# Kernel tuning notes

Hardware: AMD Instinct MI355X
Metric: run time of the kernel (lower is better)

Reference implementation:

```python
import jax, jax.numpy as jnp
import numpy as np

N = 25000      # nodes
E = 400000     # edges
D = 128        # num_hidden (per-head out dim)
H = 3          # heads
NEG_SLOPE = 0.2
BN_EPS = 1e-5


def _gatv2(x, edge_index, Wl, bl, Wr, br, att, bias):
    """PyG GATv2Conv (concat=True, add_self_loops=True, dropout=0).
    x: [N, Din]; Wl/Wr: [Din, H*D]; att: [H, D]; bias: [H*D].
    """
    n = x.shape[0]
    h, d = att.shape
    loops = jnp.arange(n)
    src = jnp.concatenate([edge_index[0], loops])  # [E+N]
    dst = jnp.concatenate([edge_index[1], loops])
    xl = (x @ Wl + bl).reshape(n, h, d)  # source transform
    xr = (x @ Wr + br).reshape(n, h, d)  # target transform
    # edge scores: a^T LeakyReLU(xl_j + xr_i)
    e = jax.nn.leaky_relu(xl[src] + xr[dst], NEG_SLOPE)   # [E+N, H, D]
    score = jnp.einsum('ehd,hd->eh', e, att)              # [E+N, H]
    # segment softmax over incoming edges of each dst node
    m = jax.ops.segment_max(score, dst, num_segments=n)   # [N, H]
    ex = jnp.exp(score - m[dst])
    denom = jax.ops.segment_sum(ex, dst, num_segments=n)  # [N, H]
    alpha = ex / denom[dst]                               # [E+N, H]
    out = jax.ops.segment_sum(alpha[:, :, None] * xl[src], dst, num_segments=n)
    return out.reshape(n, h * d) + bias                   # [N, H*D]


def _batchnorm(x, gamma, beta):
    mu = jnp.mean(x, axis=0)
    var = jnp.var(x, axis=0)  # biased, as torch BN uses for normalization
    return gamma * (x - mu) * jax.lax.rsqrt(var + BN_EPS) + beta


def setup_inputs() -> dict:
    key = jax.random.key(0)
    ks = iter(jax.random.split(key, 32))
    s = 0.1
    p = {}
    p['x'] = jax.random.normal(next(ks), (N, D), jnp.float32)
    p['edge_index'] = jax.random.randint(next(ks), (2, E), 0, N, jnp.int64)
    for i in (1, 2):
        p[f'Wl{i}'] = s * jax.random.normal(next(ks), (D, H * D), jnp.float32)
        p[f'bl{i}'] = jnp.zeros((H * D,), jnp.float32)
        p[f'Wr{i}'] = s * jax.random.normal(next(ks), (D, H * D), jnp.float32)
        p[f'br{i}'] = jnp.zeros((H * D,), jnp.float32)
        p[f'att{i}'] = s * jax.random.normal(next(ks), (H, D), jnp.float32)
        p[f'bc{i}'] = jnp.zeros((H * D,), jnp.float32)
        p[f'g{i}'] = jnp.ones((D,), jnp.float32)
        p[f'be{i}'] = jnp.zeros((D,), jnp.float32)
    p['W1'] = s * jax.random.normal(next(ks), (H * D, D), jnp.float32)
    p['b1'] = jnp.zeros((D,), jnp.float32)
    p['W2'] = s * jax.random.normal(next(ks), (2 * H * D, D), jnp.float32)
    p['b2'] = jnp.zeros((D,), jnp.float32)
    return p


def reference(x, edge_index, Wl1, bl1, Wr1, br1, att1, bc1, g1, be1,
              Wl2, bl2, Wr2, br2, att2, bc2, g2, be2, W1, b1, W2, b2):
    x_in = _gatv2(x, edge_index, Wl1, bl1, Wr1, br1, att1, bc1)  # [N, H*D]
    h = _batchnorm(x_in @ W1 + b1, g1, be1)
    h = jax.nn.relu(h)                                           # [N, D]
    h2 = _gatv2(h, edge_index, Wl2, bl2, Wr2, br2, att2, bc2)    # [N, H*D]
    out = jnp.concatenate([h2, x_in], axis=1) @ W2 + b2          # [N, D]
    out = _batchnorm(out, g2, be2)
    return jax.nn.relu(out)
```

## Files before the change

kernel.cpp:

```cpp
#include <hip/hip_runtime.h>
#include <math.h>

#define NN 25000
#define NE 400000
#define DD 128
#define HD 384
#define NEG 0.2f
#define EPS 1e-5f

typedef unsigned int u32;
typedef unsigned short u16;
typedef __attribute__((ext_vector_type(8))) short short8;
typedef __attribute__((ext_vector_type(4))) float floatx4;
typedef __attribute__((ext_vector_type(2))) float f32x2;

__device__ __forceinline__ u32 bf16_1(float x) {
    u32 u = __float_as_uint(x);
    return (u + 0x7fffu + ((u >> 16) & 1u)) >> 16;
}
__device__ __forceinline__ float blo(u32 u) { return __uint_as_float(u << 16); }
__device__ __forceinline__ float bhi(u32 u) { return __uint_as_float(u & 0xffff0000u); }

__device__ __forceinline__ void up8f2(uint4 u, f32x2* f) {
    f[0] = f32x2{blo(u.x), bhi(u.x)};
    f[1] = f32x2{blo(u.y), bhi(u.y)};
    f[2] = f32x2{blo(u.z), bhi(u.z)};
    f[3] = f32x2{blo(u.w), bhi(u.w)};
}

__device__ __forceinline__ f32x2 pk_add(f32x2 a, f32x2 b) {
    f32x2 d; asm("v_pk_add_f32 %0, %1, %2" : "=v"(d) : "v"(a), "v"(b)); return d;
}
__device__ __forceinline__ f32x2 pk_fma(f32x2 a, f32x2 b, f32x2 c) {
    f32x2 d; asm("v_pk_fma_f32 %0, %1, %2, %3" : "=v"(d) : "v"(a), "v"(b), "v"(c)); return d;
}
__device__ __forceinline__ f32x2 fabs2(f32x2 v) {
    u32 a = __float_as_uint(v.x) & 0x7fffffffu;
    u32 b = __float_as_uint(v.y) & 0x7fffffffu;
    return f32x2{__uint_as_float(a), __uint_as_float(b)};
}

__device__ __forceinline__ float row_sum16(float x) {
    int t;
    t = __builtin_amdgcn_update_dpp(0, __float_as_int(x), 0x121, 0xf, 0xf, false);
    x += __int_as_float(t);
    t = __builtin_amdgcn_update_dpp(0, __float_as_int(x), 0x122, 0xf, 0xf, false);
    x += __int_as_float(t);
    t = __builtin_amdgcn_update_dpp(0, __float_as_int(x), 0x124, 0xf, 0xf, false);
    x += __int_as_float(t);
    t = __builtin_amdgcn_update_dpp(0, __float_as_int(x), 0x128, 0xf, 0xf, false);
    x += __int_as_float(t);
    return x;
}

__global__ void k_cast_all(const float* __restrict__ x,
                           const float* __restrict__ Wl1, const float* __restrict__ Wr1,
                           const float* __restrict__ W1,
                           const float* __restrict__ Wl2, const float* __restrict__ Wr2,
                           const float* __restrict__ W2,
                           const float* __restrict__ bl1, const float* __restrict__ br1,
                           const float* __restrict__ bl2, const float* __restrict__ br2,
                           const float* __restrict__ att1, const float* __restrict__ att2,
                           const int* __restrict__ esrc, const int* __restrict__ edst,
                           u16* __restrict__ xb, u16* __restrict__ WfT1,
                           u16* __restrict__ W1T, u16* __restrict__ WfT2,
                           u16* __restrict__ W2T,
                           float* __restrict__ fb1, float* __restrict__ fb2,
                           float* __restrict__ attc1, float* __restrict__ attc2,
                           int* __restrict__ cnt, int* __restrict__ col_src,
                           float* __restrict__ stats) {
    int i = blockIdx.x * 256 + threadIdx.x;
    if (i < 400000) {
        const float4* xp = (const float4*)(x + (size_t)i * 8);
        float4 a = xp[0], b = xp[1];
        uint4 w;
        w.x = bf16_1(a.x) | (bf16_1(a.y) << 16);
        w.y = bf16_1(a.z) | (bf16_1(a.w) << 16);
        w.z = bf16_1(b.x) | (bf16_1(b.y) << 16);
        w.w = bf16_1(b.z) | (bf16_1(b.w) << 16);
        *(uint4*)(xb + (size_t)i * 8) = w;
        return;
    }
    i -= 400000;
    if (i < 400000) {
        int d = edst[i];
        int p = atomicAdd(&cnt[d], 1);
        col_src[(d << 6) + p] = esrc[i];
        return;
    }
    i -= 400000;
    if (i < 49152) { int k = i / 384, n = i - k * 384; WfT1[n * 128 + k] = (u16)bf16_1(Wl1[i]); return; }
    i -= 49152;
    if (i < 49152) { int k = i / 384, n = i - k * 384; WfT1[(384 + n) * 128 + k] = (u16)bf16_1(Wr1[i]); return; }
    i -= 49152;
    if (i < 49152) { int k = i / 128, n = i - k * 128; W1T[n * 384 + k] = (u16)bf16_1(W1[i]); return; }
    i -= 49152;
    if (i < 49152) { int k = i / 384, n = i - k * 384; WfT2[n * 128 + k] = (u16)bf16_1(Wl2[i]); return; }
    i -= 49152;
    if (i < 49152) { int k = i / 384, n = i - k * 384; WfT2[(384 + n) * 128 + k] = (u16)bf16_1(Wr2[i]); return; }
    i -= 49152;
    if (i < 98304) { int k = i / 128, n = i - k * 128; W2T[n * 768 + k] = (u16)bf16_1(W2[i]); return; }
    i -= 98304;
    if (i < 768) { fb1[i] = (i < 384) ? bl1[i] : br1[i - 384]; return; }
    i -= 768;
    if (i < 768) { fb2[i] = (i < 384) ? bl2[i] : br2[i - 384]; return; }
    i -= 768;
    if (i < 384) { attc1[i] = att1[i] * 0.86561702f; return; }
    i -= 384;
    if (i < 384) { attc2[i] = att2[i] * 0.86561702f; return; }
    i -= 384;
    if (i < 512) stats[i] = 0.f;
}
#define CAST_TOTAL (400000 + 400000 + 5 * 49152 + 98304 + 1536 + 768 + 512)

__global__ __launch_bounds__(256) void k_gemm_k128(
        const u16* __restrict__ A, const u16* __restrict__ BT,
        const float* __restrict__ bias, u16* __restrict__ Cb, int M) {
    __shared__ short sA[64 * 128];
    __shared__ short sB[128 * 128];
    int tid = threadIdx.x;
    int wv = tid >> 6, lane = tid & 63;
    int quad = lane >> 4, m16 = lane & 15;
    int mb = blockIdx.x * 64;

#pragma unroll
    for (int j = 0; j < 4; ++j) {
        int L = j * 256 + tid;
        int r = L >> 4, c8 = (L & 15) ^ (r & 15);
        int gr = mb + r; gr = gr < M ? gr : M - 1;
        __builtin_amdgcn_global_load_lds(
            (const __attribute__((address_space(1))) void*)(A + (size_t)gr * 128 + c8 * 8),
            (__attribute__((address_space(3))) void*)(sA + (size_t)L * 8), 16, 0, 0);
    }

    for (int nb6 = 0; nb6 < 6; ++nb6) {
        int nb = nb6 * 128;
        __syncthreads();
#pragma unroll
        for (int j = 0; j < 8; ++j) {
            int L = j * 256 + tid;
            int r = L >> 4, c8 = (L & 15) ^ (r & 15);
            __builtin_amdgcn_global_load_lds(
                (const __attribute__((address_space(1))) void*)(BT + (size_t)(nb + r) * 128 + c8 * 8),
                (__attribute__((address_space(3))) void*)(sB + (size_t)L * 8), 16, 0, 0);
        }
        __syncthreads();

        floatx4 acc[8];
#pragma unroll
        for (int nf = 0; nf < 8; ++nf)
#pragma unroll
            for (int r = 0; r < 4; ++r) acc[nf][r] = 0.f;

#pragma unroll
        for (int ks = 0; ks < 4; ++ks) {
            int slot = (ks * 4 + quad) ^ m16;
            short8 a0 = *(const short8*)(sA + ((size_t)(wv * 16 + m16) * 16 + slot) * 8);
#pragma unroll
            for (int nf = 0; nf < 8; ++nf) {
                short8 b = *(const short8*)(sB + ((size_t)(nf * 16 + m16) * 16 + slot) * 8);
                acc[nf] = __builtin_amdgcn_mfma_f32_16x16x32_bf16(a0, b, acc[nf], 0, 0, 0);
            }
        }
        __syncthreads();

#pragma unroll
        for (int nf = 0; nf < 8; ++nf)
#pragma unroll
            for (int r = 0; r < 4; ++r) {
                int row = wv * 16 + quad * 4 + r;
                int col = nf * 16 + m16;
                sB[row * 128 + col] = (short)bf16_1(acc[nf][r] + bias[nb + col]);
            }
        __syncthreads();

        int xr = nb >= 384;
        int h = (xr ? (nb - 384) : nb) >> 7;
        u16* cb = Cb + ((size_t)(xr * 3 + h) * NN) * 128;
#pragma unroll
        for (int i = 0; i < 4; ++i) {
            int u = i * 256 + tid;
            int row = u >> 4, c8 = u & 15;
            int grow = mb + row;
            if (grow < M)
                *(uint4*)(cb + (size_t)grow * 128 + c8 * 8) = *(const uint4*)(sB + (size_t)u * 8);
        }
    }
}

__global__ __launch_bounds__(256) void k_gemm_bf(
        const u16* __restrict__ A, const u16* __restrict__ BT,
        const float* __restrict__ bias,
        float* __restrict__ Cf, float* __restrict__ stats,
        int M, int N, int K, int lda) {
    __shared__ short smem[17408];
    short* sA = smem;
    short* sB = smem + 8192;
    int tid = threadIdx.x;
    int wv = tid >> 6, lane = tid & 63;
    int quad = lane >> 4, m16 = lane & 15;
    int mb = blockIdx.y * 64, nb = blockIdx.x * 64;

    floatx4 acc[4];
#pragma unroll
    for (int nf = 0; nf < 4; ++nf)
#pragma unroll
        for (int r = 0; r < 4; ++r) acc[nf][r] = 0.f;

    for (int k0 = 0; k0 < K; k0 += 128) {
#pragma unroll
        for (int j = 0; j < 4; ++j) {
            int L = j * 256 + tid;
            int r = L >> 4, c8 = (L & 15) ^ (r & 15);
            int gr = mb + r; gr = gr < M ? gr : M - 1;
            __builtin_amdgcn_global_load_lds(
                (const __attribute__((address_space(1))) void*)(A + (size_t)gr * lda + k0 + c8 * 8),
                (__attribute__((address_space(3))) void*)(sA + (size_t)L * 8), 16, 0, 0);
        }
#pragma unroll
        for (int j = 0; j < 4; ++j) {
            int L = j * 256 + tid;
            int r = L >> 4, c8 = (L & 15) ^ (r & 15);
            __builtin_amdgcn_global_load_lds(
                (const __attribute__((address_space(1))) void*)(BT + (size_t)(nb + r) * K + k0 + c8 * 8),
                (__attribute__((address_space(3))) void*)(sB + (size_t)L * 8), 16, 0, 0);
        }
        __syncthreads();
#pragma unroll
        for (int ks = 0; ks < 4; ++ks) {
            int slot = (ks * 4 + quad) ^ m16;
            short8 a0 = *(const short8*)(sA + ((size_t)(wv * 16 + m16) * 16 + slot) * 8);
#pragma unroll
            for (int nf = 0; nf < 4; ++nf) {
                short8 b = *(const short8*)(sB + ((size_t)(nf * 16 + m16) * 16 + slot) * 8);
                acc[nf] = __builtin_amdgcn_mfma_f32_16x16x32_bf16(a0, b, acc[nf], 0, 0, 0);
            }
        }
        __syncthreads();
    }
    float* fs = (float*)smem;
#pragma unroll
    for (int nf = 0; nf < 4; ++nf)
#pragma unroll
        for (int r = 0; r < 4; ++r) {
            int row = wv * 16 + quad * 4 + r;
            int col = nf * 16 + m16;
            fs[row * 64 + col] = acc[nf][r] + (bias ? bias[nb + col] : 0.f);
        }
    __syncthreads();
#pragma unroll
    for (int i = 0; i < 4; ++i) {
        int u = i * 256 + tid;
        int row = u >> 4, c4 = u & 15;
        int grow = mb + row;
        if (grow < M)
            *(float4*)(Cf + (size_t)grow * N + nb + c4 * 4) = *(const float4*)(fs + (size_t)u * 4);
    }
    if (stats) {
        float* ps = (float*)(smem + 16384);
        int col = tid & 63, qr = tid >> 6;
        int vr = M - mb; vr = vr < 64 ? vr : 64;
        int r0 = qr * 16, r1 = r0 + 16 < vr ? r0 + 16 : vr;
        float s = 0.f, q = 0.f;
        for (int r = r0; r < r1; ++r) { float v = fs[r * 64 + col]; s += v; q += v * v; }
        ps[qr * 64 + col] = s;
        ps[256 + qr * 64 + col] = q;
        __syncthreads();
        if (tid < 64) {
            float ss = ps[tid] + ps[64 + tid] + ps[128 + tid] + ps[192 + tid];
            atomicAdd(&stats[nb + tid], ss);
        } else if (tid < 128) {
            int c = tid - 64;
            float qq = ps[256 + c] + ps[320 + c] + ps[384 + c] + ps[448 + c];
            atomicAdd(&stats[128 + nb + c], qq);
        }
    }
}

__global__ __launch_bounds__(256) void k_gat_h(const u32* __restrict__ XLb,
                                               const u32* __restrict__ XRb,
                                               const float* __restrict__ attc,
                                               const float* __restrict__ bias,
                                               const int* __restrict__ cnt,
                                               const int* __restrict__ col_src,
                                               u32* __restrict__ outb) {
    int h = blockIdx.y;
    const u32* XLh = XLb + (size_t)h * NN * 64;
    const u32* XRh = XRb + (size_t)h * NN * 64;
    int node = blockIdx.x * 4 + (threadIdx.x >> 6);
    int lane = threadIdx.x & 63;
    int g = lane >> 4, gl = lane & 15;

    f32x2 xr2[4], a6[4], acc2[4];
    const f32x2 c23 = {0.66666667f, 0.66666667f};
    up8f2(*(const uint4*)(XRh + (size_t)node * 64 + 4 * gl), xr2);
#pragma unroll
    for (int j = 0; j < 4; ++j) {
        a6[j] = *(const f32x2*)(attc + h * 128 + 8 * gl + 2 * j);
        acc2[j] = f32x2{0.f, 0.f};
    }
    float l = 0.f;

    int e0 = node << 6;
    int cntE = cnt[node];

    int c0i = col_src[e0 + g];
    int c1i = col_src[e0 + g + 4];

    if (g == 0) {
        f32x2 xs[4];
        up8f2(*(const uint4*)(XLh + (size_t)node * 64 + 4 * gl), xs);
        f32x2 p2 = {0.f, 0.f};
#pragma unroll
        for (int j = 0; j < 4; ++j) {
            f32x2 v = pk_add(xs[j], xr2[j]);
            p2 = pk_fma(pk_fma(fabs2(v), c23, v), a6[j], p2);
        }
        float w = __builtin_amdgcn_exp2f(row_sum16(p2.x + p2.y));
        l = w;
        f32x2 w2 = {w, w};
#pragma unroll
        for (int j = 0; j < 4; ++j) acc2[j] = pk_fma(xs[j], w2, acc2[j]);
    }

    uint4 ua = *(const uint4*)(XLh + (size_t)c0i * 64 + 4 * gl);
    uint4 ub = *(const uint4*)(XLh + (size_t)c1i * 64 + 4 * gl);

    for (int t = g; t < cntE; t += 8) {
        uint4 un0 = *(const uint4*)(XLh + (size_t)col_src[e0 + t + 8] * 64 + 4 * gl);
        uint4 un1 = *(const uint4*)(XLh + (size_t)col_src[e0 + t + 12] * 64 + 4 * gl);

        f32x2 xa2[4], xb2[4];
        up8f2(ua, xa2); up8f2(ub, xb2);
        f32x2 pa2 = {0.f, 0.f}, pb2 = {0.f, 0.f};
#pragma unroll
        for (int j = 0; j < 4; ++j) {
            f32x2 va = pk_add(xa2[j], xr2[j]);
            f32x2 vb = pk_add(xb2[j], xr2[j]);
            pa2 = pk_fma(pk_fma(fabs2(va), c23, va), a6[j], pa2);
            pb2 = pk_fma(pk_fma(fabs2(vb), c23, vb), a6[j], pb2);
        }
        float pa = row_sum16(pa2.x + pa2.y);
        float pb = row_sum16(pb2.x + pb2.y);
        float wa = __builtin_amdgcn_exp2f(pa);
        float wb = ((t + 4) < cntE) ? __builtin_amdgcn_exp2f(pb) : 0.f;
        l += wa + wb;
        f32x2 wa2 = {wa, wa}, wb2 = {wb, wb};
#pragma unroll
        for (int j = 0; j < 4; ++j)
            acc2[j] = pk_fma(xa2[j], wa2, pk_fma(xb2[j], wb2, acc2[j]));

        ua = un0; ub = un1;
    }

#pragma unroll
    for (int o = 16; o <= 32; o <<= 1) {
        l += __shfl_xor(l, o);
#pragma unroll
        for (int j = 0; j < 4; ++j) {
            f32x2 s;
            s.x = __shfl_xor(acc2[j].x, o);
            s.y = __shfl_xor(acc2[j].y, o);
            acc2[j] = pk_add(acc2[j], s);
        }
    }

    if (g == 0) {
        float r = 1.f / l;
        float bv[8];
        *(float4*)&bv[0] = *(const float4*)&bias[h * 128 + 8 * gl];
        *(float4*)&bv[4] = *(const float4*)&bias[h * 128 + 8 * gl + 4];
        uint4 w;
        w.x = bf16_1(fmaf(acc2[0].x, r, bv[0])) | (bf16_1(fmaf(acc2[0].y, r, bv[1])) << 16);
        w.y = bf16_1(fmaf(acc2[1].x, r, bv[2])) | (bf16_1(fmaf(acc2[1].y, r, bv[3])) << 16);
        w.z = bf16_1(fmaf(acc2[2].x, r, bv[4])) | (bf16_1(fmaf(acc2[2].y, r, bv[5])) << 16);
        w.w = bf16_1(fmaf(acc2[3].x, r, bv[6])) | (bf16_1(fmaf(acc2[3].y, r, bv[7])) << 16);
        *(uint4*)(outb + (size_t)node * 384 + h * 64 + 4 * gl) = w;
    }
}

__global__ void k_bn_apply(float* __restrict__ y, const float* __restrict__ stats,
                           const float* __restrict__ g, const float* __restrict__ be,
                           u16* __restrict__ yb, int wf) {
    int i = blockIdx.x * 256 + threadIdx.x;
    if (i >= NN * DD / 8) return;
    int idx = i * 8;
    int c0 = idx & 127;
    float v[8];
    *(float4*)&v[0] = *(const float4*)(y + idx);
    *(float4*)&v[4] = *(const float4*)(y + idx + 4);
    const float minv = 1.f / (float)NN;
#pragma unroll
    for (int k = 0; k < 8; ++k) {
        int c = c0 + k;
        float mu = stats[c] * minv;
        float var = stats[128 + c] * minv - mu * mu;
        float sc = g[c] * rsqrtf(var + EPS);
        float sh = be[c] - mu * sc;
        v[k] = fmaxf(fmaf(v[k], sc, sh), 0.f);
    }
    if (wf) {
        *(float4*)(y + idx) = *(const float4*)&v[0];
        *(float4*)(y + idx + 4) = *(const float4*)&v[4];
    }
    if (yb) {
        uint4 w;
        w.x = bf16_1(v[0]) | (bf16_1(v[1]) << 16);
        w.y = bf16_1(v[2]) | (bf16_1(v[3]) << 16);
        w.z = bf16_1(v[4]) | (bf16_1(v[5]) << 16);
        w.w = bf16_1(v[6]) | (bf16_1(v[7]) << 16);
        *(uint4*)(yb + idx) = w;
    }
}


extern "C" void kernel_launch(void* const* d_in, const int* in_sizes, int n_in,
                              void* d_out, int out_size, void* d_ws, size_t ws_size,
                              hipStream_t stream) {
    const float* x    = (const float*)d_in[0];
    const int*   ei   = (const int*)d_in[1];
    const float* Wl1  = (const float*)d_in[2];
    const float* bl1  = (const float*)d_in[3];
    const float* Wr1  = (const float*)d_in[4];
    const float* br1  = (const float*)d_in[5];
    const float* att1 = (const float*)d_in[6];
    const float* bc1  = (const float*)d_in[7];
    const float* g1   = (const float*)d_in[8];
    const float* be1  = (const float*)d_in[9];
    const float* Wl2  = (const float*)d_in[10];
    const float* bl2  = (const float*)d_in[11];
    const float* Wr2  = (const float*)d_in[12];
    const float* br2  = (const float*)d_in[13];
    const float* att2 = (const float*)d_in[14];
    const float* bc2  = (const float*)d_in[15];
    const float* g2   = (const float*)d_in[16];
    const float* be2  = (const float*)d_in[17];
    const float* W1   = (const float*)d_in[18];
    const float* b1   = (const float*)d_in[19];
    const float* W2   = (const float*)d_in[20];
    const float* b2   = (const float*)d_in[21];
    const int* esrc = ei;
    const int* edst = ei + NE;
    float* out = (float*)d_out;

    float* bufD   = (float*)d_ws;
    float* stats  = bufD + 3200000;
    int* cnt      = (int*)(stats + 512);
    int* col_src  = cnt + 25000;
    float* fb1    = (float*)(col_src + 1600024);
    float* fb2    = fb1 + 768;
    float* attc1  = fb2 + 768;
    float* attc2  = attc1 + 384;
    u16* xb       = (u16*)(attc2 + 384);
    u16* XLb      = xb + 3200000;
    u16* XRb      = XLb + 3 * NN * 128;
    u16* bufCat   = XRb + 3 * NN * 128;
    u16* bufDb    = bufCat + 19200000;
    u16* WfT1     = bufDb + 3200000;
    u16* W1T      = WfT1 + 98304;
    u16* WfT2     = W1T + 49152;
    u16* W2T      = WfT2 + 98304;

    hipMemsetAsync(cnt, 0, NN * sizeof(int), stream);
    hipMemsetAsync(col_src, 0, (NN * 64 + 24) * sizeof(int), stream);
    k_cast_all<<<(CAST_TOTAL + 255) / 256, 256, 0, stream>>>(
        x, Wl1, Wr1, W1, Wl2, Wr2, W2, bl1, br1, bl2, br2, att1, att2, esrc, edst,
        xb, WfT1, W1T, WfT2, W2T, fb1, fb2, attc1, attc2, cnt, col_src, stats);

    dim3 blk(256);
    dim3 gK((NN + 63) / 64);
    dim3 g64(2, (NN + 63) / 64);
    dim3 gGat((NN + 3) / 4, 3);

    k_gemm_k128<<<gK, blk, 0, stream>>>(xb, WfT1, fb1, XLb, NN);
    k_gat_h<<<gGat, blk, 0, stream>>>((const u32*)XLb, (const u32*)XRb, attc1, bc1,
                                      cnt, col_src, (u32*)bufCat + 192);

    k_gemm_bf<<<g64, blk, 0, stream>>>(bufCat + 384, W1T, b1, bufD, stats, NN, DD, HD, 768);
    k_bn_apply<<<(NN * DD / 8 + 255) / 256, 256, 0, stream>>>(bufD, stats, g1, be1, bufDb, 0);

    k_gemm_k128<<<gK, blk, 0, stream>>>(bufDb, WfT2, fb2, XLb, NN);
    k_gat_h<<<gGat, blk, 0, stream>>>((const u32*)XLb, (const u32*)XRb, attc2, bc2,
                                      cnt, col_src, (u32*)bufCat);

    k_gemm_bf<<<g64, blk, 0, stream>>>(bufCat, W2T, b2, out, stats + 256, NN, DD, 768, 768);
    k_bn_apply<<<(NN * DD / 8 + 255) / 256, 256, 0, stream>>>(out, stats + 256, g2, be2, nullptr, 1);
}
```

Before: 338.3 us.

## Fuse first BatchNorm+ReLU into second projection GEMM and split GEMM over N

The standalone BN-apply kernel that wrote a bf16 copy of the hidden activations is removed. The layer-2 projection GEMM now reads fp32 pre-BN activations, applies scale/shift and ReLU, and converts to bf16 while staging the A tile into LDS. Both K=128 GEMMs also get a 2D grid that splits the 768 output columns into three 256-wide chunks per block, trading more blocks for redundant A-tile loads (and redundant BN work in the fused variant). This removes one launch and a round trip through global memory of the normalized activations.

New measurement: 330.9 us. 1.02x faster.

```diff
diff --git a/kernel.cpp b/kernel.cpp
--- a/kernel.cpp
+++ b/kernel.cpp
@@ -121,7 +121,7 @@
     int tid = threadIdx.x;
     int wv = tid >> 6, lane = tid & 63;
     int quad = lane >> 4, m16 = lane & 15;
-    int mb = blockIdx.x * 64;
+    int mb = blockIdx.y * 64;
 
 #pragma unroll
     for (int j = 0; j < 4; ++j) {
@@ -133,8 +133,107 @@
             (__attribute__((address_space(3))) void*)(sA + (size_t)L * 8), 16, 0, 0);
     }
 
-    for (int nb6 = 0; nb6 < 6; ++nb6) {
-        int nb = nb6 * 128;
+    for (int j2 = 0; j2 < 2; ++j2) {
+        int nb = blockIdx.x * 256 + j2 * 128;
+        __syncthreads();
+#pragma unroll
+        for (int j = 0; j < 8; ++j) {
+            int L = j * 256 + tid;
+            int r = L >> 4, c8 = (L & 15) ^ (r & 15);
+            __builtin_amdgcn_global_load_lds(
+                (const __attribute__((address_space(1))) void*)(BT + (size_t)(nb + r) * 128 + c8 * 8),
+                (__attribute__((address_space(3))) void*)(sB + (size_t)L * 8), 16, 0, 0);
+        }
+        __syncthreads();
+
+        floatx4 acc[8];
+#pragma unroll
+        for (int nf = 0; nf < 8; ++nf)
+#pragma unroll
+            for (int r = 0; r < 4; ++r) acc[nf][r] = 0.f;
+
+#pragma unroll
+        for (int ks = 0; ks < 4; ++ks) {
+            int slot = (ks * 4 + quad) ^ m16;
+            short8 a0 = *(const short8*)(sA + ((size_t)(wv * 16 + m16) * 16 + slot) * 8);
+#pragma unroll
+            for (int nf = 0; nf < 8; ++nf) {
+                short8 b = *(const short8*)(sB + ((size_t)(nf * 16 + m16) * 16 + slot) * 8);
+                acc[nf] = __builtin_amdgcn_mfma_f32_16x16x32_bf16(a0, b, acc[nf], 0, 0, 0);
+            }
+        }
+        __syncthreads();
+
+#pragma unroll
+        for (int nf = 0; nf < 8; ++nf)
+#pragma unroll
+            for (int r = 0; r < 4; ++r) {
+                int row = wv * 16 + quad * 4 + r;
+                int col = nf * 16 + m16;
+                sB[row * 128 + col] = (short)bf16_1(acc[nf][r] + bias[nb + col]);
+            }
+        __syncthreads();
+
+        int xr = nb >= 384;
+        int h = (xr ? (nb - 384) : nb) >> 7;
+        u16* cb = Cb + ((size_t)(xr * 3 + h) * NN) * 128;
+#pragma unroll
+        for (int i = 0; i < 4; ++i) {
+            int u = i * 256 + tid;
+            int row = u >> 4, c8 = u & 15;
+            int grow = mb + row;
+            if (grow < M)
+                *(uint4*)(cb + (size_t)grow * 128 + c8 * 8) = *(const uint4*)(sB + (size_t)u * 8);
+        }
+    }
+}
+
+__global__ __launch_bounds__(256) void k_gemm_k128_bn(
+        const float* __restrict__ Af, const float* __restrict__ stats,
+        const float* __restrict__ gg, const float* __restrict__ be,
+        const u16* __restrict__ BT,
+        const float* __restrict__ bias, u16* __restrict__ Cb, int M) {
+    __shared__ short sA[64 * 128];
+    __shared__ short sB[128 * 128];
+    int tid = threadIdx.x;
+    int wv = tid >> 6, lane = tid & 63;
+    int quad = lane >> 4, m16 = lane & 15;
+    int mb = blockIdx.y * 64;
+
+    int c8t = tid & 15;
+    const float minv = 1.f / (float)NN;
+    float sc[8], sh[8];
+#pragma unroll
+    for (int k = 0; k < 8; ++k) {
+        int c = c8t * 8 + k;
+        float mu = stats[c] * minv;
+        float var = stats[128 + c] * minv - mu * mu;
+        float s = gg[c] * rsqrtf(var + EPS);
+        sc[k] = s;
+        sh[k] = be[c] - mu * s;
+    }
+#pragma unroll
+    for (int j = 0; j < 4; ++j) {
+        int L = j * 256 + tid;
+        int r = L >> 4;
+        int gr = mb + r; gr = gr < M ? gr : M - 1;
+        const float* ap = Af + (size_t)gr * 128 + c8t * 8;
+        float4 a = *(const float4*)ap;
+        float4 b = *(const float4*)(ap + 4);
+        float v[8] = {a.x, a.y, a.z, a.w, b.x, b.y, b.z, b.w};
+        u32 pk[4];
+#pragma unroll
+        for (int k = 0; k < 4; ++k) {
+            u32 lo = bf16_1(fmaxf(fmaf(v[2 * k], sc[2 * k], sh[2 * k]), 0.f));
+            u32 hi = bf16_1(fmaxf(fmaf(v[2 * k + 1], sc[2 * k + 1], sh[2 * k + 1]), 0.f));
+            pk[k] = lo | (hi << 16);
+        }
+        uint4 w = {pk[0], pk[1], pk[2], pk[3]};
+        *(uint4*)(sA + ((size_t)(r * 16 + (c8t ^ (r & 15)))) * 8) = w;
+    }
+
+    for (int j2 = 0; j2 < 2; ++j2) {
+        int nb = blockIdx.x * 256 + j2 * 128;
         __syncthreads();
 #pragma unroll
         for (int j = 0; j < 8; ++j) {
@@ -455,8 +554,7 @@
     u16* XLb      = xb + 3200000;
     u16* XRb      = XLb + 3 * NN * 128;
     u16* bufCat   = XRb + 3 * NN * 128;
-    u16* bufDb    = bufCat + 19200000;
-    u16* WfT1     = bufDb + 3200000;
+    u16* WfT1     = bufCat + 19200000;
     u16* W1T      = WfT1 + 98304;
     u16* WfT2     = W1T + 49152;
     u16* W2T      = WfT2 + 98304;
@@ -468,7 +566,7 @@
         xb, WfT1, W1T, WfT2, W2T, fb1, fb2, attc1, attc2, cnt, col_src, stats);
 
     dim3 blk(256);
-    dim3 gK((NN + 63) / 64);
+    dim3 gK(3, (NN + 63) / 64);
     dim3 g64(2, (NN + 63) / 64);
     dim3 gGat((NN + 3) / 4, 3);
 
@@ -477,9 +575,8 @@
                                       cnt, col_src, (u32*)bufCat + 192);
 
     k_gemm_bf<<<g64, blk, 0, stream>>>(bufCat + 384, W1T, b1, bufD, stats, NN, DD, HD, 768);
-    k_bn_apply<<<(NN * DD / 8 + 255) / 256, 256, 0, stream>>>(bufD, stats, g1, be1, bufDb, 0);
-
-    k_gemm_k128<<<gK, blk, 0, stream>>>(bufDb, WfT2, fb2, XLb, NN);
+
+    k_gemm_k128_bn<<<gK, blk, 0, stream>>>(bufD, stats, g1, be1, WfT2, fb2, XLb, NN);
     k_gat_h<<<gGat, blk, 0, stream>>>((const u32*)XLb, (const u32*)XRb, attc2, bc2,
                                       cnt, col_src, (u32*)bufCat);
 
```
